# Performance work log

Measured on AMD Instinct MI355X. Metric: run time of the kernel, lower is better.

The kernel has to match this reference:

```python
import jax, jax.numpy as jnp
import numpy as np

B, C = 131072, 64
GAMMA = 2.0
CORR_WEIGHT = 0.5
CORR_THRESH = 0.3


def setup_inputs() -> dict:
    key = jax.random.key(0)
    k1, k2, k3 = jax.random.split(key, 3)
    inputs = jax.random.normal(k1, (B, C), dtype=jnp.float32)
    targets = jax.random.randint(k2, (B, C), 0, 2).astype(jnp.float32)
    pos_weights = jax.random.uniform(k3, (C,), dtype=jnp.float32, minval=1.0, maxval=5.0)
    return {"inputs": inputs, "targets": targets, "pos_weights": pos_weights}


def reference(inputs, targets, pos_weights):
    b, c = inputs.shape
    # label_correlation buffer is None at first forward -> equals batch correlation
    corr = jnp.matmul(targets.T, targets) / b  # [C, C]

    probs = jax.nn.sigmoid(inputs)
    p_t = probs * targets + (1.0 - probs) * (1.0 - targets)
    focal_weight = (1.0 - p_t) ** GAMMA

    # BCE-with-logits with pos_weight, stable via log_sigmoid
    bce = -(pos_weights * targets * jax.nn.log_sigmoid(inputs)
            + (1.0 - targets) * jax.nn.log_sigmoid(-inputs))
    focal_loss = focal_weight * bce

    # Vectorized correlation penalty.
    # Original loop: penalty[b,i] = cw * sum_{j!=i, corr[i,j]>0.3}
    #     t_i * t_j * |pred_i - pred_j| * corr[i,j]
    # With binary preds: |p_i - p_j| = p_i + p_j - 2 p_i p_j
    pred = (probs >= 0.5).astype(inputs.dtype)
    off_diag = ~jnp.eye(c, dtype=bool)
    A = jnp.where((corr > CORR_THRESH) & off_diag, corr, 0.0) * CORR_WEIGHT  # [C,C]
    tA = jnp.matmul(targets, A.T)            # [B,C] : sum_j A[i,j] * t_j
    tpA = jnp.matmul(targets * pred, A.T)    # [B,C] : sum_j A[i,j] * t_j * p_j
    penalty = targets * (pred * tA + tpA - 2.0 * pred * tpA)

    return jnp.mean(focal_loss + penalty)
```

## Files before the change

kernel.cpp:

```cpp
#include <hip/hip_runtime.h>

#define NROWS 131072
#define NCOLS 64
#define SBLK 2048
#define STHR 256
#define GBLK 512
#define GTHR 256
#define FNBLK 512
#define FNTHR 512
#define FNWAVES 8


__global__ __launch_bounds__(STHR, 6)
void kernS(const float* __restrict__ in, const float* __restrict__ tg,
           const float* __restrict__ pw, unsigned* __restrict__ Mmv,
           float* __restrict__ pkF, uint4* __restrict__ gZero) {
    __shared__ unsigned ldsM[4][64];
    __shared__ float fp[4];
    const int tid = threadIdx.x;
    if (blockIdx.x == 0) {
        const uint4 z4 = {0u, 0u, 0u, 0u};
#pragma unroll
        for (int k = 0; k < 8; ++k) gZero[tid + k * STHR] = z4;
    }
    const int gtid = blockIdx.x * STHR + tid;
    const int lane = tid & 63;
    const int wv = tid >> 6;
    const int h = lane >> 4;
    const int c4 = (lane & 15) * 4;
    const int jc = c4 + h;

    const float4 pwv = *reinterpret_cast<const float4*>(pw + c4);
    const float4 pwm1 = {pwv.x - 1.f, pwv.y - 1.f, pwv.z - 1.f, pwv.w - 1.f};
    const float4* in4 = reinterpret_cast<const float4*>(in);
    const float4* tg4 = reinterpret_cast<const float4*>(tg);

    float4 xr[4], tr[4];
#pragma unroll
    for (int k = 0; k < 4; ++k) xr[k] = in4[(size_t)gtid + (size_t)k * (SBLK * STHR)];
#pragma unroll
    for (int k = 0; k < 4; ++k) tr[k] = tg4[(size_t)gtid + (size_t)k * (SBLK * STHR)];

    float fsum = 0.f;
    unsigned m4[4] = {0u, 0u, 0u, 0u};
    unsigned v4[4] = {0u, 0u, 0u, 0u};
    const unsigned hbit = 1u << h;

    auto elem = [&](float x, float t, float pm1, unsigned bq, unsigned& mk, unsigned& vk) {
        const float s2l = __builtin_fmaf(t, 2.8853900817779268f, -1.4426950408889634f);
        const float z2 = x * s2l;
        const float e = exp2f(-fabsf(z2));
        const float d = 1.f + e;
        const float r = __builtin_amdgcn_rcpf(d);
        const float core = __log2f(d) + fmaxf(-z2, 0.f);
        const bool pos = z2 >= 0.f;
        const float w = pos ? e * r : r;
        const float wt = __builtin_fmaf(t, pm1, 1.f);
        fsum = __builtin_fmaf(w * w * core, wt, fsum);
        const bool tb = t > 0.5f;
        mk |= tb ? bq : 0u;
        vk |= (tb && pos) ? bq : 0u;
    };

#pragma unroll
    for (int k = 0; k < 4; ++k) {
        const unsigned bq = hbit << (4 * k);
        elem(xr[k].x, tr[k].x, pwm1.x, bq, m4[0], v4[0]);
        elem(xr[k].y, tr[k].y, pwm1.y, bq, m4[1], v4[1]);
        elem(xr[k].z, tr[k].z, pwm1.z, bq, m4[2], v4[2]);
        elem(xr[k].w, tr[k].w, pwm1.w, bq, m4[3], v4[3]);
    }
    fsum *= 0.6931471805599453f;

#pragma unroll
    for (int k = 0; k < 4; ++k) {
        m4[k] |= __shfl_xor(m4[k], 16, 64);
        m4[k] |= __shfl_xor(m4[k], 32, 64);
        v4[k] |= __shfl_xor(v4[k], 16, 64);
        v4[k] |= __shfl_xor(v4[k], 32, 64);
    }
    const unsigned m = (h & 2) ? ((h & 1) ? m4[3] : m4[2]) : ((h & 1) ? m4[1] : m4[0]);
    const unsigned v = (h & 2) ? ((h & 1) ? v4[3] : v4[2]) : ((h & 1) ? v4[1] : v4[0]);

    ldsM[wv][jc] = (m & 0xFFFFu) | (v << 16);

#pragma unroll
    for (int off = 32; off; off >>= 1) fsum += __shfl_down(fsum, off, 64);
    if (lane == 0) fp[wv] = fsum;
    __syncthreads();

    if (tid == 0) pkF[blockIdx.x] = fp[0] + fp[1] + fp[2] + fp[3];

    const int d = tid >> 7;
    const int col = (tid >> 1) & 63;
    const int sel = tid & 1;
    const unsigned a = ldsM[2 * d][col];
    const unsigned b = ldsM[2 * d + 1][col];
    const unsigned m32 = (a & 0xFFFFu) | (b << 16);
    const unsigned v32 = (a >> 16) | (b & 0xFFFF0000u);
    Mmv[((size_t)(blockIdx.x * 2 + d) * 64 + col) * 2 + sel] = sel ? v32 : m32;
}

__global__ __launch_bounds__(GTHR, 8)
void kernG(const unsigned* __restrict__ Mmv,
           unsigned* __restrict__ gS, unsigned* __restrict__ gP) {
    const int tid = threadIdx.x;
    const int lane = tid & 63;
    const int gw = blockIdx.x * (GTHR / 64) + (tid >> 6);
    const int i0 = (gw >> 6) * 2;
    const int w0 = (gw & 63) * 64;
    const uint2* p = reinterpret_cast<const uint2*>(Mmv) + (size_t)w0 * 64 + lane;

    unsigned S0 = 0u, S1 = 0u, P0 = 0u, P1 = 0u;
#pragma unroll 8
    for (int t = 0; t < 64; ++t) {
        const uint2 mv = p[(size_t)t * 64];
        const unsigned wm = mv.x & ~mv.y;
        const unsigned mi0 = (unsigned)__builtin_amdgcn_readlane((int)mv.x, i0);
        const unsigned vi0 = (unsigned)__builtin_amdgcn_readlane((int)mv.y, i0);
        const unsigned mi1 = (unsigned)__builtin_amdgcn_readlane((int)mv.x, i0 + 1);
        const unsigned vi1 = (unsigned)__builtin_amdgcn_readlane((int)mv.y, i0 + 1);
        S0 += (unsigned)__popc(mi0 & mv.x);
        P0 += (unsigned)__popc(vi0 & wm);
        S1 += (unsigned)__popc(mi1 & mv.x);
        P1 += (unsigned)__popc(vi1 & wm);
    }
    atomicAdd(&gS[i0 * 64 + lane], S0);
    atomicAdd(&gS[(i0 + 1) * 64 + lane], S1);
    atomicAdd(&gP[i0 * 64 + lane], P0);
    atomicAdd(&gP[(i0 + 1) * 64 + lane], P1);
}

__global__ __launch_bounds__(1024)
void kernBC(const unsigned* __restrict__ gS, const unsigned* __restrict__ gP,
            const float* __restrict__ pkF, float* __restrict__ out) {
    const int tid = threadIdx.x;
    double acc = 0.0;
#pragma unroll
    for (int kk = 0; kk < 4; ++kk) {
        const int c = tid + kk * 1024;
        const unsigned S = gS[c], P = gP[c];
        const int i = c >> 6, j = c & 63;
        const float corr = (float)S * (1.0f / (float)NROWS);
        if (i != j && corr > 0.3f) acc += (double)corr * (double)P;
    }
    acc += (double)pkF[tid] + (double)pkF[tid + 1024];
#pragma unroll
    for (int off = 32; off; off >>= 1) acc += __shfl_down(acc, off, 64);
    __shared__ double wred[16];
    const int lane = tid & 63, wv = tid >> 6;
    if (lane == 0) wred[wv] = acc;
    __syncthreads();
    if (tid < 16) {
        double tot = wred[tid];
#pragma unroll
        for (int off = 8; off; off >>= 1) tot += __shfl_down(tot, off, 64);
        if (tid == 0)
            out[0] = (float)(tot * (1.0 / (double)((size_t)NROWS * NCOLS)));
    }
}

__global__ __launch_bounds__(FNTHR, 2)
void kernAfb(const float* __restrict__ in, const float* __restrict__ tg,
             const float* __restrict__ pw, float* __restrict__ pkF,
             unsigned* __restrict__ gS, unsigned* __restrict__ gP) {
    __shared__ unsigned maskbuf[FNWAVES][64][2];
    __shared__ float fpart[FNWAVES];
    const int tid = threadIdx.x;
    const int lane = tid & 63;
    const int wv = tid >> 6;
    const int h = lane >> 4;
    const int c4 = (lane & 15) * 4;
    const int jc = c4 + h;
    const int row0 = blockIdx.x * (FNWAVES * 32) + wv * 32;

    const float4 pw4 = *reinterpret_cast<const float4*>(pw + c4);
    const float4* inp = reinterpret_cast<const float4*>(in)
                        + (size_t)(row0 + h) * 16 + (lane & 15);
    const float4* tgp = reinterpret_cast<const float4*>(tg)
                        + (size_t)(row0 + h) * 16 + (lane & 15);
    float4 xr[8], tr[8];
#pragma unroll
    for (int q = 0; q < 8; ++q) xr[q] = inp[(size_t)q * 64];
#pragma unroll
    for (int q = 0; q < 8; ++q) tr[q] = tgp[(size_t)q * 64];

    float fsum = 0.f;
    unsigned m4[4] = {0u, 0u, 0u, 0u};
    unsigned v4[4] = {0u, 0u, 0u, 0u};
    const unsigned hbit = 1u << h;
    auto elem = [&](float x, float t, float pwc, unsigned bq, unsigned& mk, unsigned& vk) {
        float ax = fabsf(x);
        float e = __expf(-ax);
        float L = __logf(1.f + e);
        float inv = __builtin_amdgcn_rcpf(1.f + e);
        float qq = e * inv;
        bool tb = t > 0.5f;
        bool pb = x >= 0.f;
        float w = (tb == pb) ? qq : inv;
        float bce = tb ? pwc * (L + fmaxf(-x, 0.f)) : (L + fmaxf(x, 0.f));
        fsum += w * w * bce;
        mk |= tb ? bq : 0u;
        vk |= (tb && pb) ? bq : 0u;
    };
#pragma unroll
    for (int q = 0; q < 8; ++q) {
        const unsigned bq = hbit << (4 * q);
        elem(xr[q].x, tr[q].x, pw4.x, bq, m4[0], v4[0]);
        elem(xr[q].y, tr[q].y, pw4.y, bq, m4[1], v4[1]);
        elem(xr[q].z, tr[q].z, pw4.z, bq, m4[2], v4[2]);
        elem(xr[q].w, tr[q].w, pw4.w, bq, m4[3], v4[3]);
    }
#pragma unroll
    for (int k = 0; k < 4; ++k) {
        m4[k] |= __shfl_xor(m4[k], 16, 64);
        m4[k] |= __shfl_xor(m4[k], 32, 64);
        v4[k] |= __shfl_xor(v4[k], 16, 64);
        v4[k] |= __shfl_xor(v4[k], 32, 64);
    }
    const unsigned m = (h & 2) ? ((h & 1) ? m4[3] : m4[2]) : ((h & 1) ? m4[1] : m4[0]);
    const unsigned v = (h & 2) ? ((h & 1) ? v4[3] : v4[2]) : ((h & 1) ? v4[1] : v4[0]);
    maskbuf[wv][jc][0] = m;
    maskbuf[wv][jc][1] = v;
#pragma unroll
    for (int off = 32; off; off >>= 1) fsum += __shfl_down(fsum, off, 64);
    if (lane == 0) fpart[wv] = fsum;
    __syncthreads();
    if (tid == 0) {
        float tot = 0.f;
#pragma unroll
        for (int k = 0; k < FNWAVES; ++k) tot += fpart[k];
        pkF[blockIdx.x] = tot;
    }
    unsigned aS[8] = {0u,0u,0u,0u,0u,0u,0u,0u};
    unsigned aP[8] = {0u,0u,0u,0u,0u,0u,0u,0u};
    const int a0 = wv * 8;
#pragma unroll
    for (int ww = 0; ww < FNWAVES; ++ww) {
        const unsigned mw = maskbuf[ww][lane][0];
        const unsigned vw = maskbuf[ww][lane][1];
        const unsigned wmw = mw & ~vw;
#pragma unroll
        for (int r = 0; r < 8; ++r) {
            const unsigned mi = maskbuf[ww][a0 + r][0];
            const unsigned vi = maskbuf[ww][a0 + r][1];
            aS[r] += (unsigned)__popc(mi & mw);
            aP[r] += (unsigned)__popc(vi & wmw);
        }
    }
#pragma unroll
    for (int r = 0; r < 8; ++r) {
        atomicAdd(&gS[(a0 + r) * 64 + lane], aS[r]);
        atomicAdd(&gP[(a0 + r) * 64 + lane], aP[r]);
    }
}

__global__ __launch_bounds__(1024)
void kernWfb(const unsigned* __restrict__ gS, const unsigned* __restrict__ gP,
             const float* __restrict__ pkF, float* __restrict__ out) {
    const int tid = threadIdx.x;
    double acc = 0.0;
#pragma unroll
    for (int kk = 0; kk < 4; ++kk) {
        const int c = tid + kk * 1024;
        const unsigned S = gS[c], P = gP[c];
        const int i = c >> 6, j = c & 63;
        const float corr = (float)S * (1.0f / (float)NROWS);
        if (i != j && corr > 0.3f) acc += (double)corr * (double)P;
    }
    if (tid < FNBLK) acc += (double)pkF[tid];
#pragma unroll
    for (int off = 32; off; off >>= 1) acc += __shfl_down(acc, off, 64);
    __shared__ double wred[16];
    const int lane = tid & 63, wv = tid >> 6;
    if (lane == 0) wred[wv] = acc;
    __syncthreads();
    if (tid < 16) {
        double tot = wred[tid];
#pragma unroll
        for (int off = 8; off; off >>= 1) tot += __shfl_down(tot, off, 64);
        if (tid == 0)
            out[0] = (float)(tot * (1.0 / (double)((size_t)NROWS * NCOLS)));
    }
}

extern "C" void kernel_launch(void* const* d_in, const int* in_sizes, int n_in,
                              void* d_out, int out_size, void* d_ws, size_t ws_size,
                              hipStream_t stream) {
    const float* in = (const float*)d_in[0];
    const float* tg = (const float*)d_in[1];
    const float* pw = (const float*)d_in[2];
    float* out = (float*)d_out;
    char* ws = (char*)d_ws;

    float* pkF = (float*)ws;
    unsigned* gS = (unsigned*)(ws + 8192);
    unsigned* gP = (unsigned*)(ws + 24576);
    unsigned* Mmv = (unsigned*)(ws + 65536);
    const size_t need = 65536 + (size_t)4096 * 64 * 2 * sizeof(unsigned);

    if (ws_size >= need) {
        kernS<<<SBLK, STHR, 0, stream>>>(in, tg, pw, Mmv, pkF, (uint4*)gS);
        kernG<<<GBLK, GTHR, 0, stream>>>(Mmv, gS, gP);
        kernBC<<<1, 1024, 0, stream>>>(gS, gP, pkF, out);
    } else {
        hipMemsetAsync(ws + 8192, 0, 32768, stream);
        kernAfb<<<FNBLK, FNTHR, 0, stream>>>(in, tg, pw, pkF, gS, gP);
        kernWfb<<<1, 1024, 0, stream>>>(gS, gP, pkF, out);
    }
}
```

Before: 29.40 us.

## Fuse final reduction into kernG via last-block counter and pack elementwise math

Removes the separate single-block finalize kernel by having the last kernG block (detected with an atomic counter and fences) compute the correlation-weighted penalty sum and write the output. The counter is zeroed in kernS by extending the workspace zeroing. The kernS focal-loss math is restructured into 2-wide float vectors to allow packed FP32 ops and drops the abs/branch form, using exp2(z) directly. The unclamped form can overflow for very large logits, and the extra atomic and fence add a small cost to every kernG block.

Result: slower. 59.08 us (+100.9%).

```diff
diff --git a/kernel.cpp b/kernel.cpp
--- a/kernel.cpp
+++ b/kernel.cpp
@@ -10,6 +10,8 @@
 #define FNTHR 512
 #define FNWAVES 8
 
+typedef __attribute__((ext_vector_type(2))) float f32x2;
+
 
 __global__ __launch_bounds__(STHR, 6)
 void kernS(const float* __restrict__ in, const float* __restrict__ tg,
@@ -21,7 +23,7 @@
     if (blockIdx.x == 0) {
         const uint4 z4 = {0u, 0u, 0u, 0u};
 #pragma unroll
-        for (int k = 0; k < 8; ++k) gZero[tid + k * STHR] = z4;
+        for (int k = 0; k < 9; ++k) gZero[tid + k * STHR] = z4;
     }
     const int gtid = blockIdx.x * STHR + tid;
     const int lane = tid & 63;
@@ -31,7 +33,8 @@
     const int jc = c4 + h;
 
     const float4 pwv = *reinterpret_cast<const float4*>(pw + c4);
-    const float4 pwm1 = {pwv.x - 1.f, pwv.y - 1.f, pwv.z - 1.f, pwv.w - 1.f};
+    const f32x2 pmA = {pwv.x - 1.f, pwv.y - 1.f};
+    const f32x2 pmB = {pwv.z - 1.f, pwv.w - 1.f};
     const float4* in4 = reinterpret_cast<const float4*>(in);
     const float4* tg4 = reinterpret_cast<const float4*>(tg);
 
@@ -41,36 +44,40 @@
 #pragma unroll
     for (int k = 0; k < 4; ++k) tr[k] = tg4[(size_t)gtid + (size_t)k * (SBLK * STHR)];
 
-    float fsum = 0.f;
+    f32x2 facc = {0.f, 0.f};
     unsigned m4[4] = {0u, 0u, 0u, 0u};
     unsigned v4[4] = {0u, 0u, 0u, 0u};
     const unsigned hbit = 1u << h;
 
-    auto elem = [&](float x, float t, float pm1, unsigned bq, unsigned& mk, unsigned& vk) {
-        const float s2l = __builtin_fmaf(t, 2.8853900817779268f, -1.4426950408889634f);
-        const float z2 = x * s2l;
-        const float e = exp2f(-fabsf(z2));
-        const float d = 1.f + e;
-        const float r = __builtin_amdgcn_rcpf(d);
-        const float core = __log2f(d) + fmaxf(-z2, 0.f);
-        const bool pos = z2 >= 0.f;
-        const float w = pos ? e * r : r;
-        const float wt = __builtin_fmaf(t, pm1, 1.f);
-        fsum = __builtin_fmaf(w * w * core, wt, fsum);
-        const bool tb = t > 0.5f;
-        mk |= tb ? bq : 0u;
-        vk |= (tb && pos) ? bq : 0u;
+    auto pair = [&](float x0, float x1, float t0, float t1, f32x2 pm1,
+                    unsigned bq, unsigned& mk0, unsigned& vk0,
+                    unsigned& mk1, unsigned& vk1) {
+        const f32x2 xv = {x0, x1};
+        const f32x2 tv = {t0, t1};
+        const f32x2 s2l = tv * 2.8853900817779268f - 1.4426950408889634f;
+        const f32x2 z2 = xv * s2l;
+        f32x2 e2, w, lg;
+        e2.x = exp2f(z2.x);  e2.y = exp2f(z2.y);
+        const f32x2 d2 = e2 + 1.f;
+        w.x = __builtin_amdgcn_rcpf(d2.x);  w.y = __builtin_amdgcn_rcpf(d2.y);
+        lg.x = __log2f(d2.x);  lg.y = __log2f(d2.y);
+        const f32x2 core = lg - z2;
+        const f32x2 wt = tv * pm1 + 1.f;
+        const f32x2 w2c = (w * w) * core;
+        facc = w2c * wt + facc;
+        const bool tb0 = t0 > 0.5f, tb1 = t1 > 0.5f;
+        const bool p0 = z2.x >= 0.f, p1 = z2.y >= 0.f;
+        mk0 |= tb0 ? bq : 0u;  vk0 |= (tb0 && p0) ? bq : 0u;
+        mk1 |= tb1 ? bq : 0u;  vk1 |= (tb1 && p1) ? bq : 0u;
     };
 
 #pragma unroll
     for (int k = 0; k < 4; ++k) {
         const unsigned bq = hbit << (4 * k);
-        elem(xr[k].x, tr[k].x, pwm1.x, bq, m4[0], v4[0]);
-        elem(xr[k].y, tr[k].y, pwm1.y, bq, m4[1], v4[1]);
-        elem(xr[k].z, tr[k].z, pwm1.z, bq, m4[2], v4[2]);
-        elem(xr[k].w, tr[k].w, pwm1.w, bq, m4[3], v4[3]);
-    }
-    fsum *= 0.6931471805599453f;
+        pair(xr[k].x, xr[k].y, tr[k].x, tr[k].y, pmA, bq, m4[0], v4[0], m4[1], v4[1]);
+        pair(xr[k].z, xr[k].w, tr[k].z, tr[k].w, pmB, bq, m4[2], v4[2], m4[3], v4[3]);
+    }
+    float fsum = (facc.x + facc.y) * 0.6931471805599453f;
 
 #pragma unroll
     for (int k = 0; k < 4; ++k) {
@@ -103,7 +110,9 @@
 
 __global__ __launch_bounds__(GTHR, 8)
 void kernG(const unsigned* __restrict__ Mmv,
-           unsigned* __restrict__ gS, unsigned* __restrict__ gP) {
+           unsigned* __restrict__ gS, unsigned* __restrict__ gP,
+           const float* __restrict__ pkF, unsigned* __restrict__ cnt,
+           float* __restrict__ out) {
     const int tid = threadIdx.x;
     const int lane = tid & 63;
     const int gw = blockIdx.x * (GTHR / 64) + (tid >> 6);
@@ -129,35 +138,34 @@
     atomicAdd(&gS[(i0 + 1) * 64 + lane], S1);
     atomicAdd(&gP[i0 * 64 + lane], P0);
     atomicAdd(&gP[(i0 + 1) * 64 + lane], P1);
-}
-
-__global__ __launch_bounds__(1024)
-void kernBC(const unsigned* __restrict__ gS, const unsigned* __restrict__ gP,
-            const float* __restrict__ pkF, float* __restrict__ out) {
-    const int tid = threadIdx.x;
+
+    __threadfence();
+    __shared__ int isLast;
+    if (tid == 0) isLast = (atomicAdd(cnt, 1u) == GBLK - 1) ? 1 : 0;
+    __syncthreads();
+    if (!isLast) return;
+    __threadfence();
+
     double acc = 0.0;
 #pragma unroll
-    for (int kk = 0; kk < 4; ++kk) {
-        const int c = tid + kk * 1024;
+    for (int kk = 0; kk < 16; ++kk) {
+        const int c = tid + kk * GTHR;
         const unsigned S = gS[c], P = gP[c];
         const int i = c >> 6, j = c & 63;
         const float corr = (float)S * (1.0f / (float)NROWS);
         if (i != j && corr > 0.3f) acc += (double)corr * (double)P;
     }
-    acc += (double)pkF[tid] + (double)pkF[tid + 1024];
+#pragma unroll
+    for (int kk = 0; kk < 8; ++kk)
+        acc += (double)pkF[tid + kk * GTHR];
 #pragma unroll
     for (int off = 32; off; off >>= 1) acc += __shfl_down(acc, off, 64);
-    __shared__ double wred[16];
-    const int lane = tid & 63, wv = tid >> 6;
-    if (lane == 0) wred[wv] = acc;
-    __syncthreads();
-    if (tid < 16) {
-        double tot = wred[tid];
-#pragma unroll
-        for (int off = 8; off; off >>= 1) tot += __shfl_down(tot, off, 64);
-        if (tid == 0)
-            out[0] = (float)(tot * (1.0 / (double)((size_t)NROWS * NCOLS)));
-    }
+    __shared__ double wred[4];
+    if (lane == 0) wred[tid >> 6] = acc;
+    __syncthreads();
+    if (tid == 0)
+        out[0] = (float)((wred[0] + wred[1] + wred[2] + wred[3])
+                         * (1.0 / (double)((size_t)NROWS * NCOLS)));
 }
 
 __global__ __launch_bounds__(FNTHR, 2)
@@ -296,13 +304,13 @@
     float* pkF = (float*)ws;
     unsigned* gS = (unsigned*)(ws + 8192);
     unsigned* gP = (unsigned*)(ws + 24576);
+    unsigned* cnt = (unsigned*)(ws + 40960);
     unsigned* Mmv = (unsigned*)(ws + 65536);
     const size_t need = 65536 + (size_t)4096 * 64 * 2 * sizeof(unsigned);
 
     if (ws_size >= need) {
         kernS<<<SBLK, STHR, 0, stream>>>(in, tg, pw, Mmv, pkF, (uint4*)gS);
-        kernG<<<GBLK, GTHR, 0, stream>>>(Mmv, gS, gP);
-        kernBC<<<1, 1024, 0, stream>>>(gS, gP, pkF, out);
+        kernG<<<GBLK, GTHR, 0, stream>>>(Mmv, gS, gP, pkF, cnt, out);
     } else {
         hipMemsetAsync(ws + 8192, 0, 32768, stream);
         kernAfb<<<FNBLK, FNTHR, 0, stream>>>(in, tg, pw, pkF, gS, gP);
```
